# Kernel optimization log

Hardware: AMD Instinct MI355X
Metric: run time of the kernel (lower is better)

## Reference

```python
import jax, jax.numpy as jnp
import numpy as np


def sparsemax(z, axis=0):
    # Standard sparsemax projection onto the simplex (Martins & Astudillo 2016).
    n = z.shape[axis]
    # shift by max for numerical stability (invariant for sparsemax)
    z = z - jnp.max(z, axis=axis, keepdims=True)
    z_sorted = -jnp.sort(-z, axis=axis)  # descending sort along axis
    z_cumsum = jnp.cumsum(z_sorted, axis=axis)
    k_shape = [1] * z.ndim
    k_shape[axis] = n
    k = jnp.arange(1, n + 1, dtype=z.dtype).reshape(k_shape)
    support = (1.0 + k * z_sorted) > z_cumsum  # in-support mask
    k_sup = jnp.sum(support, axis=axis, keepdims=True)  # support size (int)
    # cumsum value at index k_sup-1 along axis
    cs_k = jnp.take_along_axis(z_cumsum, k_sup - 1, axis=axis)
    tau = (cs_k - 1.0) / k_sup.astype(z.dtype)
    return jnp.maximum(z - tau, 0.0)


def setup_inputs() -> dict:
    key = jax.random.key(0)
    k_x, k_a = jax.random.split(key)
    x = jax.random.normal(k_x, (4096, 8192), dtype=jnp.float32)
    a = jnp.asarray(1.0, dtype=jnp.float32)  # nn.Parameter initialized to 1.0
    return {"x": x, "a": a}


def reference(x, a):
    z = -jnp.exp(a) * x
    return sparsemax(z, axis=0)
```

## Files before the change

### kernel.cpp

```cpp
#include <hip/hip_runtime.h>
#include <math.h>


constexpr int ROWS = 4096;
constexpr int COLS = 8192;
constexpr int CAP  = 64;

constexpr int CB = 32;
constexpr int RB = 512;
constexpr int T1 = 512;
constexpr int KK = RB / 64;

__global__ __launch_bounds__(T1, 4)
void k1_gather(const float* __restrict__ x, const float* __restrict__ a,
               int* __restrict__ cnt, float* __restrict__ cand)
{
    __shared__ float wmax[8][33];
    __shared__ float mcol[CB];

    const int tid  = threadIdx.x;
    const int cq   = tid & 7;
    const int rg   = tid >> 3;
    const int lane = tid & 63;
    const int wave = tid >> 6;

    const int  colb = blockIdx.x * CB;
    const long col  = colb + cq * 4;
    const int  row0 = blockIdx.y * RB;
    const float s   = -expf(a[0]);

    float z[KK][4];
#pragma unroll
    for (int k = 0; k < KK; ++k) {
        const long row = row0 + rg + k * 64;
        const float4 v = *reinterpret_cast<const float4*>(x + row * COLS + col);
        z[k][0] = s * v.x; z[k][1] = s * v.y;
        z[k][2] = s * v.z; z[k][3] = s * v.w;
    }
#pragma unroll
    for (int k = 0; k < KK; ++k)
        asm volatile("" : "+v"(z[k][0]), "+v"(z[k][1]),
                          "+v"(z[k][2]), "+v"(z[k][3]));

    float pm[4] = {z[0][0], z[0][1], z[0][2], z[0][3]};
#pragma unroll
    for (int k = 1; k < KK; ++k)
#pragma unroll
        for (int c = 0; c < 4; ++c) pm[c] = fmaxf(pm[c], z[k][c]);
#pragma unroll
    for (int m = 8; m < 64; m <<= 1)
#pragma unroll
        for (int c = 0; c < 4; ++c) pm[c] = fmaxf(pm[c], __shfl_xor(pm[c], m, 64));
    if (lane < 8) {
#pragma unroll
        for (int c = 0; c < 4; ++c) wmax[wave][lane * 4 + c] = pm[c];
    }
    __syncthreads();
    if (tid < CB) {
        float m = wmax[0][tid];
#pragma unroll
        for (int w = 1; w < 8; ++w) m = fmaxf(m, wmax[w][tid]);
        mcol[tid] = m;
    }
    __syncthreads();

    float thr[4];
#pragma unroll
    for (int c = 0; c < 4; ++c) thr[c] = mcol[cq * 4 + c] - 1.0f;
#pragma unroll
    for (int k = 0; k < KK; ++k)
#pragma unroll
        for (int c = 0; c < 4; ++c) {
            const float v = z[k][c];
            if (v > thr[c]) {
                const int ci  = colb + cq * 4 + c;
                const int idx = atomicAdd(&cnt[ci], 1);
                if (idx < CAP) cand[(long)ci * CAP + idx] = v;
            }
        }
}

__global__ __launch_bounds__(256)
void k2_solve(const int* __restrict__ cnt, const float* __restrict__ cand,
              const float* __restrict__ x, const float* __restrict__ a,
              float* __restrict__ tau)
{
    const int lane = threadIdx.x & 63;
    const int wave = threadIdx.x >> 6;
    const int col  = blockIdx.x * 4 + wave;
    const int K    = cnt[col];

    float t = -3.0e38f;
    if (K <= CAP) {
        const float v = (lane < K) ? cand[(long)col * CAP + lane] : -3.3e38f;
        float prev = 0.f;
        for (int it = 0; it < CAP + 2; ++it) {
            const bool act = v > t;
            float ssum = act ? v : 0.f;
            float scnt = act ? 1.f : 0.f;
#pragma unroll
            for (int m = 1; m < 64; m <<= 1) {
                ssum += __shfl_xor(ssum, m, 64);
                scnt += __shfl_xor(scnt, m, 64);
            }
            t = (ssum - 1.0f) / scnt;
            if (scnt == prev) break;
            prev = scnt;
        }
    } else {
        const float s = -expf(a[0]);
        float prev = 0.f;
        for (int it = 0; it < 256; ++it) {
            float ssum = 0.f, scnt = 0.f;
            for (int i = 0; i < ROWS / 64; ++i) {
                const float zz = s * x[(long)(lane + i * 64) * COLS + col];
                if (zz > t) { ssum += zz; scnt += 1.f; }
            }
#pragma unroll
            for (int m = 1; m < 64; m <<= 1) {
                ssum += __shfl_xor(ssum, m, 64);
                scnt += __shfl_xor(scnt, m, 64);
            }
            t = (ssum - 1.0f) / scnt;
            if (scnt == prev) break;
            prev = scnt;
        }
    }
    if (lane == 0) tau[col] = t;
}

__global__ __launch_bounds__(256, 8)
void k3_epilogue(const float* __restrict__ x, const float* __restrict__ a,
                 const float* __restrict__ tau, float* __restrict__ out)
{
    const float s = -expf(a[0]);
    const float4* x4 = reinterpret_cast<const float4*>(x);
    const float4* t4 = reinterpret_cast<const float4*>(tau);
    float4*       o4 = reinterpret_cast<float4*>(out);
    const int N4 = ROWS * (COLS / 4);
    const int stride = gridDim.x * blockDim.x;
    for (int i = blockIdx.x * blockDim.x + threadIdx.x; i < N4; i += stride) {
        const float4 v  = x4[i];
        const float4 tt = t4[i & (COLS / 4 - 1)];
        float4 o;
        o.x = fmaxf(fmaf(s, v.x, -tt.x), 0.f);
        o.y = fmaxf(fmaf(s, v.y, -tt.y), 0.f);
        o.z = fmaxf(fmaf(s, v.z, -tt.z), 0.f);
        o.w = fmaxf(fmaf(s, v.w, -tt.w), 0.f);
        o4[i] = o;
    }
}

extern "C" void kernel_launch(void* const* d_in, const int* in_sizes, int n_in,
                              void* d_out, int out_size, void* d_ws, size_t ws_size,
                              hipStream_t stream) {
    const float* x = (const float*)d_in[0];
    const float* a = (const float*)d_in[1];
    float* out = (float*)d_out;

    char*  ws   = (char*)d_ws;
    int*   cnt  = (int*)ws;
    float* tau  = (float*)(ws + 32 * 1024);
    float* cand = (float*)(ws + 64 * 1024);

    hipMemsetAsync(cnt, 0, COLS * sizeof(int), stream);
    hipLaunchKernelGGL(k1_gather, dim3(COLS / CB, ROWS / RB), dim3(T1), 0, stream,
                       x, a, cnt, cand);
    hipLaunchKernelGGL(k2_solve, dim3(COLS / 4), dim3(256), 0, stream,
                       cnt, cand, x, a, tau);
    hipLaunchKernelGGL(k3_epilogue, dim3(2048), dim3(256), 0, stream,
                       x, a, tau, out);
}
```

Baseline: 264.5 us.

## Restructure candidate gather into per-rowblock local-atomic slots, drop memset, nontemporal stores

The first kernel now has each thread stream a 64-row by 4-column strip twice: a max pass, then a filter pass that re-reads the data, presumably from cache. Candidates are counted with shared-memory atomics into per-(rowblock, column) slots instead of global atomics, which also removes the memset. The solve kernel merges 16 rowblocks times 12 slots per column. The epilogue uses nontemporal stores for the output. This trades global atomic contention for a second read of x, and a small per-block cap raises the risk of falling back to the slow full-column path.

```diff
diff --git a/kernel.cpp b/kernel.cpp
--- a/kernel.cpp
+++ b/kernel.cpp
@@ -4,126 +4,137 @@
 
 constexpr int ROWS = 4096;
 constexpr int COLS = 8192;
-constexpr int CAP  = 64;
 
-constexpr int CB = 32;
-constexpr int RB = 512;
-constexpr int T1 = 512;
-constexpr int KK = RB / 64;
+constexpr int CB   = 256;
+constexpr int RB   = 256;
+constexpr int T1   = 256;
+constexpr int SUBR = RB / 4;
+constexpr int NRB  = ROWS / RB;
+constexpr int NCB  = COLS / CB;
+constexpr int CAP  = 12;
+constexpr int SLOTS = NRB * CAP;
 
-__global__ __launch_bounds__(T1, 4)
-void k1_gather(const float* __restrict__ x, const float* __restrict__ a,
-               int* __restrict__ cnt, float* __restrict__ cand)
+typedef float vfloat4 __attribute__((ext_vector_type(4)));
+
+__global__ __launch_bounds__(T1, 2)
+void k1_maxfilter(const float* __restrict__ x, const float* __restrict__ a,
+                  int* __restrict__ ccnt, float* __restrict__ cand)
 {
-    __shared__ float wmax[8][33];
-    __shared__ float mcol[CB];
+    __shared__ float smax[4][CB];
+    __shared__ float thrS[CB];
+    __shared__ int   lcnt[CB];
 
-    const int tid  = threadIdx.x;
-    const int cq   = tid & 7;
-    const int rg   = tid >> 3;
-    const int lane = tid & 63;
-    const int wave = tid >> 6;
+    const int tid = threadIdx.x;
+    const int l   = tid & 63;
+    const int sub = tid >> 6;
 
     const int  colb = blockIdx.x * CB;
-    const long col  = colb + cq * 4;
-    const int  row0 = blockIdx.y * RB;
+    const int  row0 = blockIdx.y * RB + sub * SUBR;
+    const long base = (long)row0 * COLS + colb + 4 * l;
     const float s   = -expf(a[0]);
 
-    float z[KK][4];
-#pragma unroll
-    for (int k = 0; k < KK; ++k) {
-        const long row = row0 + rg + k * 64;
-        const float4 v = *reinterpret_cast<const float4*>(x + row * COLS + col);
-        z[k][0] = s * v.x; z[k][1] = s * v.y;
-        z[k][2] = s * v.z; z[k][3] = s * v.w;
+    float pm0 = -3e38f, pm1 = -3e38f, pm2 = -3e38f, pm3 = -3e38f;
+#pragma unroll 8
+    for (int k = 0; k < SUBR; ++k) {
+        const float4 v = *reinterpret_cast<const float4*>(x + base + (long)k * COLS);
+        pm0 = fmaxf(pm0, s * v.x);
+        pm1 = fmaxf(pm1, s * v.y);
+        pm2 = fmaxf(pm2, s * v.z);
+        pm3 = fmaxf(pm3, s * v.w);
     }
-#pragma unroll
-    for (int k = 0; k < KK; ++k)
-        asm volatile("" : "+v"(z[k][0]), "+v"(z[k][1]),
-                          "+v"(z[k][2]), "+v"(z[k][3]));
-
-    float pm[4] = {z[0][0], z[0][1], z[0][2], z[0][3]};
-#pragma unroll
-    for (int k = 1; k < KK; ++k)
-#pragma unroll
-        for (int c = 0; c < 4; ++c) pm[c] = fmaxf(pm[c], z[k][c]);
-#pragma unroll
-    for (int m = 8; m < 64; m <<= 1)
-#pragma unroll
-        for (int c = 0; c < 4; ++c) pm[c] = fmaxf(pm[c], __shfl_xor(pm[c], m, 64));
-    if (lane < 8) {
-#pragma unroll
-        for (int c = 0; c < 4; ++c) wmax[wave][lane * 4 + c] = pm[c];
-    }
+    smax[sub][4 * l + 0] = pm0;
+    smax[sub][4 * l + 1] = pm1;
+    smax[sub][4 * l + 2] = pm2;
+    smax[sub][4 * l + 3] = pm3;
     __syncthreads();
-    if (tid < CB) {
-        float m = wmax[0][tid];
-#pragma unroll
-        for (int w = 1; w < 8; ++w) m = fmaxf(m, wmax[w][tid]);
-        mcol[tid] = m;
+    {
+        float m = fmaxf(fmaxf(smax[0][tid], smax[1][tid]),
+                        fmaxf(smax[2][tid], smax[3][tid]));
+        thrS[tid] = m - 1.0f;
+        lcnt[tid] = 0;
     }
     __syncthreads();
 
-    float thr[4];
-#pragma unroll
-    for (int c = 0; c < 4; ++c) thr[c] = mcol[cq * 4 + c] - 1.0f;
-#pragma unroll
-    for (int k = 0; k < KK; ++k)
-#pragma unroll
-        for (int c = 0; c < 4; ++c) {
-            const float v = z[k][c];
-            if (v > thr[c]) {
-                const int ci  = colb + cq * 4 + c;
-                const int idx = atomicAdd(&cnt[ci], 1);
-                if (idx < CAP) cand[(long)ci * CAP + idx] = v;
-            }
-        }
+    const float t0 = thrS[4 * l + 0];
+    const float t1 = thrS[4 * l + 1];
+    const float t2 = thrS[4 * l + 2];
+    const float t3 = thrS[4 * l + 3];
+    const long  slotbase = (long)blockIdx.y * CAP;
+    for (int k = 0; k < SUBR; ++k) {
+        const float4 v = *reinterpret_cast<const float4*>(x + base + (long)k * COLS);
+        const float z0 = s * v.x, z1 = s * v.y, z2 = s * v.z, z3 = s * v.w;
+        if (z0 > t0) { int i = atomicAdd(&lcnt[4*l+0], 1);
+                       if (i < CAP) cand[(long)(colb+4*l+0) * SLOTS + slotbase + i] = z0; }
+        if (z1 > t1) { int i = atomicAdd(&lcnt[4*l+1], 1);
+                       if (i < CAP) cand[(long)(colb+4*l+1) * SLOTS + slotbase + i] = z1; }
+        if (z2 > t2) { int i = atomicAdd(&lcnt[4*l+2], 1);
+                       if (i < CAP) cand[(long)(colb+4*l+2) * SLOTS + slotbase + i] = z2; }
+        if (z3 > t3) { int i = atomicAdd(&lcnt[4*l+3], 1);
+                       if (i < CAP) cand[(long)(colb+4*l+3) * SLOTS + slotbase + i] = z3; }
+    }
+    __syncthreads();
+    ccnt[blockIdx.y * COLS + colb + tid] = lcnt[tid];
 }
 
-__global__ __launch_bounds__(256)
-void k2_solve(const int* __restrict__ cnt, const float* __restrict__ cand,
+__global__ __launch_bounds__(256, 4)
+void k2_solve(const int* __restrict__ ccnt, const float* __restrict__ cand,
               const float* __restrict__ x, const float* __restrict__ a,
               float* __restrict__ tau)
 {
     const int lane = threadIdx.x & 63;
-    const int wave = threadIdx.x >> 6;
-    const int col  = blockIdx.x * 4 + wave;
-    const int K    = cnt[col];
+    const int wv   = threadIdx.x >> 6;
+    const int col  = blockIdx.x * 4 + wv;
+
+    bool ovf = false;
+    float v0 = -3.3e38f, v1 = -3.3e38f, v2 = -3.3e38f;
+    {
+        const int s0 = lane, s1 = lane + 64, s2 = lane + 128;
+        const int n0 = ccnt[(s0 / CAP) * COLS + col];
+        const int n1 = ccnt[(s1 / CAP) * COLS + col];
+        const int n2 = ccnt[(s2 / CAP) * COLS + col];
+        ovf = (n0 > CAP) | (n1 > CAP) | (n2 > CAP);
+        const float c0 = cand[(long)col * SLOTS + s0];
+        const float c1 = cand[(long)col * SLOTS + s1];
+        const float c2 = cand[(long)col * SLOTS + s2];
+        if ((s0 % CAP) < n0) v0 = c0;
+        if ((s1 % CAP) < n1) v1 = c1;
+        if ((s2 % CAP) < n2) v2 = c2;
+    }
 
     float t = -3.0e38f;
-    if (K <= CAP) {
-        const float v = (lane < K) ? cand[(long)col * CAP + lane] : -3.3e38f;
+    if (!__any(ovf)) {
         float prev = 0.f;
-        for (int it = 0; it < CAP + 2; ++it) {
-            const bool act = v > t;
-            float ssum = act ? v : 0.f;
-            float scnt = act ? 1.f : 0.f;
+        for (int it = 0; it < 200; ++it) {
+            float ss = 0.f, sc = 0.f;
+            if (v0 > t) { ss += v0; sc += 1.f; }
+            if (v1 > t) { ss += v1; sc += 1.f; }
+            if (v2 > t) { ss += v2; sc += 1.f; }
 #pragma unroll
             for (int m = 1; m < 64; m <<= 1) {
-                ssum += __shfl_xor(ssum, m, 64);
-                scnt += __shfl_xor(scnt, m, 64);
+                ss += __shfl_xor(ss, m, 64);
+                sc += __shfl_xor(sc, m, 64);
             }
-            t = (ssum - 1.0f) / scnt;
-            if (scnt == prev) break;
-            prev = scnt;
+            t = (ss - 1.0f) / sc;
+            if (sc == prev) break;
+            prev = sc;
         }
     } else {
         const float s = -expf(a[0]);
         float prev = 0.f;
         for (int it = 0; it < 256; ++it) {
-            float ssum = 0.f, scnt = 0.f;
+            float ss = 0.f, sc = 0.f;
             for (int i = 0; i < ROWS / 64; ++i) {
                 const float zz = s * x[(long)(lane + i * 64) * COLS + col];
-                if (zz > t) { ssum += zz; scnt += 1.f; }
+                if (zz > t) { ss += zz; sc += 1.f; }
             }
 #pragma unroll
             for (int m = 1; m < 64; m <<= 1) {
-                ssum += __shfl_xor(ssum, m, 64);
-                scnt += __shfl_xor(scnt, m, 64);
+                ss += __shfl_xor(ss, m, 64);
+                sc += __shfl_xor(sc, m, 64);
             }
-            t = (ssum - 1.0f) / scnt;
-            if (scnt == prev) break;
-            prev = scnt;
+            t = (ss - 1.0f) / sc;
+            if (sc == prev) break;
+            prev = sc;
         }
     }
     if (lane == 0) tau[col] = t;
@@ -134,20 +145,20 @@
                  const float* __restrict__ tau, float* __restrict__ out)
 {
     const float s = -expf(a[0]);
-    const float4* x4 = reinterpret_cast<const float4*>(x);
-    const float4* t4 = reinterpret_cast<const float4*>(tau);
-    float4*       o4 = reinterpret_cast<float4*>(out);
+    const float4*  x4 = reinterpret_cast<const float4*>(x);
+    const float4*  t4 = reinterpret_cast<const float4*>(tau);
+    vfloat4*       o4 = reinterpret_cast<vfloat4*>(out);
     const int N4 = ROWS * (COLS / 4);
     const int stride = gridDim.x * blockDim.x;
     for (int i = blockIdx.x * blockDim.x + threadIdx.x; i < N4; i += stride) {
         const float4 v  = x4[i];
         const float4 tt = t4[i & (COLS / 4 - 1)];
-        float4 o;
+        vfloat4 o;
         o.x = fmaxf(fmaf(s, v.x, -tt.x), 0.f);
         o.y = fmaxf(fmaf(s, v.y, -tt.y), 0.f);
         o.z = fmaxf(fmaf(s, v.z, -tt.z), 0.f);
         o.w = fmaxf(fmaf(s, v.w, -tt.w), 0.f);
-        o4[i] = o;
+        __builtin_nontemporal_store(o, &o4[i]);
     }
 }
 
@@ -159,15 +170,14 @@
     float* out = (float*)d_out;
 
     char*  ws   = (char*)d_ws;
-    int*   cnt  = (int*)ws;
-    float* tau  = (float*)(ws + 32 * 1024);
-    float* cand = (float*)(ws + 64 * 1024);
+    int*   ccnt = (int*)ws;
+    float* tau  = (float*)(ws + 512 * 1024);
+    float* cand = (float*)(ws + 1024 * 1024);
 
-    hipMemsetAsync(cnt, 0, COLS * sizeof(int), stream);
-    hipLaunchKernelGGL(k1_gather, dim3(COLS / CB, ROWS / RB), dim3(T1), 0, stream,
-                       x, a, cnt, cand);
+    hipLaunchKernelGGL(k1_maxfilter, dim3(NCB, NRB), dim3(T1), 0, stream,
+                       x, a, ccnt, cand);
     hipLaunchKernelGGL(k2_solve, dim3(COLS / 4), dim3(256), 0, stream,
-                       cnt, cand, x, a, tau);
+                       ccnt, cand, x, a, tau);
     hipLaunchKernelGGL(k3_epilogue, dim3(2048), dim3(256), 0, stream,
                        x, a, tau, out);
 }
```

Result: slower. 451.5 us (+70.7%).
